# Kernel tuning notes

Hardware: AMD Instinct MI355X
Metric: run time of the kernel (lower is better)

The kernel has to match this reference:

```python
import jax, jax.numpy as jnp
import numpy as np

DIM = 1024
NUM_HEADS = 16


def setup_inputs() -> dict:
    key = jax.random.key(0)
    ks = jax.random.split(key, 8)
    B, N, C = 2, 2048, DIM
    x = jax.random.normal(ks[0], (B, N, C), dtype=jnp.float32)
    attn_mask = jnp.zeros((B, 1, N, N), dtype=jnp.float32)
    # learned parameters
    w_qkv = jax.random.normal(ks[1], (3 * C, C), dtype=jnp.float32) * (C ** -0.5)
    q_bias = jnp.zeros((C,), dtype=jnp.float32)
    k_bias = jnp.zeros((C,), dtype=jnp.float32)
    v_bias = jnp.zeros((C,), dtype=jnp.float32)
    w_proj = jax.random.normal(ks[2], (C, C), dtype=jnp.float32) * (C ** -0.5)
    b_proj = jnp.zeros((C,), dtype=jnp.float32)
    return {
        "x": x, "attn_mask": attn_mask,
        "w_qkv": w_qkv, "q_bias": q_bias, "k_bias": k_bias, "v_bias": v_bias,
        "w_proj": w_proj, "b_proj": b_proj,
        "num_heads": NUM_HEADS,
    }


def reference(x, attn_mask, w_qkv, q_bias, k_bias, v_bias, w_proj, b_proj, num_heads):
    B, N, C = x.shape
    H = num_heads
    hd = C // H
    scale = hd ** -0.5
    alpha = 32.0
    # fused qkv projection with concatenated biases
    qkv_bias = jnp.concatenate([q_bias, k_bias, v_bias])
    qkv = x @ w_qkv.T + qkv_bias                       # [B, N, 3C]
    qkv = qkv.reshape(B, N, 3, H, hd).transpose(2, 0, 3, 1, 4)  # [3, B, H, N, hd]
    q, k, v = qkv[0], qkv[1], qkv[2]
    # stabilization trick: scale q down by alpha, compute scores, re-scale after max-subtraction
    q = q * (scale / alpha)
    attn = jnp.einsum('bhld,bhmd->bhlm', q, k)         # [B, H, N, N]
    attn = (attn - jnp.max(attn, axis=-1, keepdims=True)) * alpha
    attn = attn + attn_mask                            # additive mask, broadcast over heads
    attn = jax.nn.softmax(attn, axis=-1)
    out = jnp.einsum('bhlm,bhmd->blhd', attn, v).reshape(B, N, C)
    out = out @ w_proj.T + b_proj
    return out
```

## Files before the change

kernel.cpp:

```cpp
#include <hip/hip_runtime.h>

typedef unsigned short u16;
typedef __bf16   bf16x8 __attribute__((ext_vector_type(8)));
typedef float    f32x4  __attribute__((ext_vector_type(4)));
typedef unsigned u32x4v __attribute__((ext_vector_type(4)));
typedef u16      u16x8  __attribute__((ext_vector_type(8)));

#define DEV __device__ __forceinline__

DEV u16 f2bf(float f) {
  unsigned u = __float_as_uint(f);
  u += 0x7fffu + ((u >> 16) & 1u);
  return (u16)(u >> 16);
}

DEV f32x4 fzero() { f32x4 z; z[0]=0.f; z[1]=0.f; z[2]=0.f; z[3]=0.f; return z; }

DEV void async_cp16(void* lds, const void* g) {
  __builtin_amdgcn_global_load_lds(
      (const __attribute__((address_space(1))) void*)g,
      (__attribute__((address_space(3))) void*)lds, 16, 0, 0);
}

__global__ void k_cvt_bf16(const float* __restrict__ in, u16* __restrict__ out, int n8) {
  int i = blockIdx.x * blockDim.x + threadIdx.x;
  if (i >= n8) return;
  const float4* in4 = (const float4*)in;
  float4 a = in4[2*i], b = in4[2*i+1];
  u16x8 r;
  r[0]=f2bf(a.x); r[1]=f2bf(a.y); r[2]=f2bf(a.z); r[3]=f2bf(a.w);
  r[4]=f2bf(b.x); r[5]=f2bf(b.y); r[6]=f2bf(b.z); r[7]=f2bf(b.w);
  *(u16x8*)(out + 8*(size_t)i) = r;
}

__global__ void k_zero_flag(unsigned* f) {
  if (threadIdx.x == 0 && blockIdx.x == 0) *f = 0u;
}

__global__ void k_mask_or(const u32x4v* __restrict__ m, int n4, unsigned* __restrict__ f) {
  unsigned o = 0;
  int stride = gridDim.x * blockDim.x;
  for (int i = blockIdx.x * blockDim.x + threadIdx.x; i < n4; i += stride) {
    u32x4v v = m[i];
    o |= v[0] | v[1] | v[2] | v[3];
  }
  if (o & 0x7fffffffu) atomicOr(f, 1u);
}

template<int EPI>
__global__ __launch_bounds__(256)
void k_gemm_nt(const u16* __restrict__ A, const u16* __restrict__ B,
               int N, int K, int nbn,
               const float* __restrict__ bq, const float* __restrict__ bk,
               const float* __restrict__ bv,
               u16* __restrict__ qo, u16* __restrict__ ko, u16* __restrict__ vto,
               float* __restrict__ fo, const float* __restrict__ bp)
{
  __shared__ u16 sA[2][4096];
  __shared__ u16 sB[2][4096];

  const int tid  = threadIdx.x;
  const int lane = tid & 63;
  const int wave = tid >> 6;
  const int lr = lane & 15, lg = lane >> 4;
  const int wr = wave >> 1, wc = wave & 1;

  const int per = gridDim.x >> 3;
  const int bid = blockIdx.x;
  const int swz = (bid & 7) * per + (bid >> 3);
  const int bm0 = (swz / nbn) << 7;
  const int bn0 = (swz - (swz / nbn) * nbn) << 7;

  const size_t Kb = (size_t)K * 2;

  auto stage = [&](int buf, int kt) {
#pragma unroll
    for (int j = 0; j < 2; ++j) {
      int off = (tid + j * 256) << 4;
      int row = off >> 6;
      int ch  = (off & 63) >> 4;
      int gch = ch ^ (row & 3);
      async_cp16((char*)&sA[buf][0] + off,
                 (const char*)A + (size_t)(bm0 + row) * Kb + (size_t)kt * 64 + gch * 16);
      async_cp16((char*)&sB[buf][0] + off,
                 (const char*)B + (size_t)(bn0 + row) * Kb + (size_t)kt * 64 + gch * 16);
    }
  };

  f32x4 acc[4][4];
#pragma unroll
  for (int i = 0; i < 4; ++i)
#pragma unroll
    for (int j = 0; j < 4; ++j) acc[i][j] = fzero();

  const int nk = K >> 5;
  stage(0, 0);
  __syncthreads();

  for (int kt = 0; kt < nk; ++kt) {
    const int cur = kt & 1;
    if (kt + 1 < nk) stage(cur ^ 1, kt + 1);

    bf16x8 af[4], bfr[4];
#pragma unroll
    for (int mi = 0; mi < 4; ++mi) {
      int row = (wr << 6) + (mi << 4) + lr;
      int addr = (row << 6) + ((lg ^ (row & 3)) << 4);
      af[mi] = *(const bf16x8*)((const char*)&sA[cur][0] + addr);
    }
#pragma unroll
    for (int ni = 0; ni < 4; ++ni) {
      int row = (wc << 6) + (ni << 4) + lr;
      int addr = (row << 6) + ((lg ^ (row & 3)) << 4);
      bfr[ni] = *(const bf16x8*)((const char*)&sB[cur][0] + addr);
    }
#pragma unroll
    for (int mi = 0; mi < 4; ++mi)
#pragma unroll
      for (int ni = 0; ni < 4; ++ni)
        acc[mi][ni] = __builtin_amdgcn_mfma_f32_16x16x32_bf16(af[mi], bfr[ni], acc[mi][ni], 0, 0, 0);

    __syncthreads();
  }

#pragma unroll
  for (int mi = 0; mi < 4; ++mi) {
#pragma unroll
    for (int ni = 0; ni < 4; ++ni) {
      int col = bn0 + (wc << 6) + (ni << 4) + lr;
      if (EPI == 0) {
        int s = col >> 10, hd = col & 1023;
        int h = hd >> 6, d = hd & 63;
        float bias = (s == 0 ? bq[hd] : (s == 1 ? bk[hd] : bv[hd]));
#pragma unroll
        for (int r = 0; r < 4; ++r) {
          int m = bm0 + (wr << 6) + (mi << 4) + (lg << 2) + r;
          int b = m >> 11, n = m & 2047;
          u16 val = f2bf(acc[mi][ni][r] + bias);
          size_t bh = (size_t)(b * 16 + h);
          if (s == 0)      qo[(bh * 2048 + n) * 64 + d] = val;
          else if (s == 1) ko[(bh * 2048 + n) * 64 + d] = val;
          else             vto[(bh * 64 + d) * 2048 + n] = val;
        }
      } else {
        float bias = bp[col];
#pragma unroll
        for (int r = 0; r < 4; ++r) {
          int m = bm0 + (wr << 6) + (mi << 4) + (lg << 2) + r;
          fo[(size_t)m * N + col] = acc[mi][ni][r] + bias;
        }
      }
    }
  }
}

__global__ __launch_bounds__(256)
void k_attn(const u16* __restrict__ qb, const u16* __restrict__ kb,
            const u16* __restrict__ vtb, u16* __restrict__ ao,
            const float* __restrict__ mask, const unsigned* __restrict__ flag)
{
  constexpr int N = 2048, D = 64;
  __shared__ u16 sK[2][4096];
  __shared__ u16 sV[2][4096];

  const int tid  = threadIdx.x;
  const int lane = tid & 63;
  const int wave = tid >> 6;
  const int lr = lane & 15, lg = lane >> 4;

  const int bid  = blockIdx.x;
  const int xcd  = bid & 7, slot = bid >> 3;
  const int bh   = xcd + 8 * (slot >> 5);
  const int qt   = slot & 31;
  const int b    = bh >> 4, h = bh & 15;

  const u16* Kbh = kb  + (size_t)bh * N * D;
  const u16* Vbh = vtb + (size_t)bh * D * N;
  const int q_lo = qt * 64 + wave * 16;
  const int qg   = q_lo + lr;

  bf16x8 qf[2];
  {
    const u16* qrow = qb + ((size_t)bh * N + qg) * D;
    qf[0] = *(const bf16x8*)(qrow + lg * 8);
    qf[1] = *(const bf16x8*)(qrow + 32 + lg * 8);
  }

  const unsigned use_mask = *flag;
  const float* maskb = mask + (size_t)b * N * N;

  float m_run = -INFINITY, lsum = 0.f;
  f32x4 o[4];
#pragma unroll
  for (int i = 0; i < 4; ++i) o[i] = fzero();

  auto stage = [&](int buf, int kt) {
#pragma unroll
    for (int j = 0; j < 2; ++j) {
      int off = (tid + j * 256) << 4;
      int row = off >> 7;
      int ch  = (off & 127) >> 4;
      int gch = ch ^ (row & 7);
      async_cp16((char*)&sK[buf][0] + off,
                 (const char*)Kbh + (size_t)(kt * 64 + row) * 128 + gch * 16);
      async_cp16((char*)&sV[buf][0] + off,
                 (const char*)Vbh + (size_t)row * (N * 2) + (size_t)kt * 128 + gch * 16);
    }
  };

  stage(0, 0);
  __syncthreads();

  const float SCALE = 0.125f;
  const float L2E   = 1.44269504088896340736f;

  for (int kt = 0; kt < N / 64; ++kt) {
    const int cur = kt & 1;
    if (kt + 1 < N / 64) stage(cur ^ 1, kt + 1);

    f32x4 sc[4];
#pragma unroll
    for (int mi = 0; mi < 4; ++mi) sc[mi] = fzero();
#pragma unroll
    for (int mi = 0; mi < 4; ++mi)
#pragma unroll
      for (int ks = 0; ks < 2; ++ks) {
        int row = (mi << 4) + lr;
        int addr = (row << 7) + ((((ks << 2) + lg) ^ (row & 7)) << 4);
        bf16x8 kf = *(const bf16x8*)((const char*)&sK[cur][0] + addr);
        sc[mi] = __builtin_amdgcn_mfma_f32_16x16x32_bf16(kf, qf[ks], sc[mi], 0, 0, 0);
      }

    float t[4][4];
#pragma unroll
    for (int mi = 0; mi < 4; ++mi)
#pragma unroll
      for (int r = 0; r < 4; ++r) t[mi][r] = sc[mi][r] * SCALE;

    if (use_mask) {
#pragma unroll
      for (int mi = 0; mi < 4; ++mi)
#pragma unroll
        for (int r = 0; r < 4; ++r) {
          int kg = kt * 64 + (mi << 4) + (lg << 2) + r;
          t[mi][r] += maskb[(size_t)qg * N + kg];
        }
    }

    float pm = t[0][0];
#pragma unroll
    for (int mi = 0; mi < 4; ++mi)
#pragma unroll
      for (int r = 0; r < 4; ++r) pm = fmaxf(pm, t[mi][r]);
    pm = fmaxf(pm, __shfl_xor(pm, 16, 64));
    pm = fmaxf(pm, __shfl_xor(pm, 32, 64));

    const float m_new = fmaxf(m_run, pm);
    const float f = __builtin_amdgcn_exp2f((m_run - m_new) * L2E);
    m_run = m_new;

    float p[4][4];
    float rs = 0.f;
#pragma unroll
    for (int mi = 0; mi < 4; ++mi)
#pragma unroll
      for (int r = 0; r < 4; ++r) {
        p[mi][r] = __builtin_amdgcn_exp2f((t[mi][r] - m_new) * L2E);
        rs += p[mi][r];
      }
    rs += __shfl_xor(rs, 16, 64);
    rs += __shfl_xor(rs, 32, 64);
    lsum = lsum * f + rs;

    {
      float fr[4];
#pragma unroll
      for (int r = 0; r < 4; ++r) fr[r] = __shfl(f, (lg << 2) + r, 64);
#pragma unroll
      for (int ni = 0; ni < 4; ++ni)
#pragma unroll
        for (int r = 0; r < 4; ++r) o[ni][r] *= fr[r];
    }

    unsigned P32[4][2];
#pragma unroll
    for (int mi = 0; mi < 4; ++mi)
#pragma unroll
      for (int rp = 0; rp < 2; ++rp) {
        unsigned lo = f2bf(p[mi][2 * rp]);
        unsigned hi = f2bf(p[mi][2 * rp + 1]);
        P32[mi][rp] = lo | (hi << 16);
      }

    bf16x8 pf[2];
#pragma unroll
    for (int ks = 0; ks < 2; ++ks) {
      u32x4v w;
#pragma unroll
      for (int wd = 0; wd < 4; ++wd) {
        int src = lr + ((((lg << 1) + (wd >> 1)) & 3) << 4);
        unsigned vlo = __shfl(P32[2 * ks + 0][wd & 1], src, 64);
        unsigned vhi = __shfl(P32[2 * ks + 1][wd & 1], src, 64);
        w[wd] = (lg & 2) ? vhi : vlo;
      }
      pf[ks] = __builtin_bit_cast(bf16x8, w);
    }

#pragma unroll
    for (int ni = 0; ni < 4; ++ni)
#pragma unroll
      for (int ks = 0; ks < 2; ++ks) {
        int drow = (ni << 4) + lr;
        int addr = (drow << 7) + ((((ks << 2) + lg) ^ (drow & 7)) << 4);
        bf16x8 vf = *(const bf16x8*)((const char*)&sV[cur][0] + addr);
        o[ni] = __builtin_amdgcn_mfma_f32_16x16x32_bf16(pf[ks], vf, o[ni], 0, 0, 0);
      }

    __syncthreads();
  }

  const float inv = 1.0f / lsum;
  float ivr[4];
#pragma unroll
  for (int r = 0; r < 4; ++r) ivr[r] = __shfl(inv, (lg << 2) + r, 64);

#pragma unroll
  for (int ni = 0; ni < 4; ++ni) {
    int d = (ni << 4) + lr;
#pragma unroll
    for (int r = 0; r < 4; ++r) {
      int qrow = q_lo + (lg << 2) + r;
      ao[((size_t)(b * N + qrow)) * 1024 + h * 64 + d] = f2bf(o[ni][r] * ivr[r]);
    }
  }
}

extern "C" void kernel_launch(void* const* d_in, const int* in_sizes, int n_in,
                              void* d_out, int out_size, void* d_ws, size_t ws_size,
                              hipStream_t stream) {
  const float* x      = (const float*)d_in[0];
  const float* mask   = (const float*)d_in[1];
  const float* w_qkv  = (const float*)d_in[2];
  const float* q_bias = (const float*)d_in[3];
  const float* k_bias = (const float*)d_in[4];
  const float* v_bias = (const float*)d_in[5];
  const float* w_proj = (const float*)d_in[6];
  const float* b_proj = (const float*)d_in[7];
  float* out = (float*)d_out;

  const int B = 2, N = 2048, C = 1024;
  const int M = B * N;

  u16* ws     = (u16*)d_ws;
  u16* xb     = ws;
  u16* wqkvb  = ws + 4194304;
  u16* wprojb = ws + 7340032;
  u16* qbuf   = ws + 8388608;
  u16* kbuf   = ws + 12582912;
  u16* vtbuf  = ws + 16777216;
  unsigned* flag = (unsigned*)(ws + 20971520);
  u16* aob    = xb;

  k_cvt_bf16<<<(M * C / 8 + 255) / 256, 256, 0, stream>>>(x, xb, M * C / 8);
  k_cvt_bf16<<<(3 * C * C / 8 + 255) / 256, 256, 0, stream>>>(w_qkv, wqkvb, 3 * C * C / 8);
  k_cvt_bf16<<<(C * C / 8 + 255) / 256, 256, 0, stream>>>(w_proj, wprojb, C * C / 8);

  k_zero_flag<<<1, 64, 0, stream>>>(flag);
  k_mask_or<<<1024, 256, 0, stream>>>((const u32x4v*)mask, B * N * N / 4, flag);

  k_gemm_nt<0><<<(M / 128) * (3 * C / 128), 256, 0, stream>>>(
      xb, wqkvb, 3 * C, C, 3 * C / 128,
      q_bias, k_bias, v_bias, qbuf, kbuf, vtbuf, nullptr, nullptr);

  k_attn<<<B * 16 * (N / 64), 256, 0, stream>>>(qbuf, kbuf, vtbuf, aob, mask, flag);

  k_gemm_nt<1><<<(M / 128) * (C / 128), 256, 0, stream>>>(
      aob, wprojb, C, C, C / 128,
      nullptr, nullptr, nullptr, nullptr, nullptr, nullptr, out, b_proj);
}
```

Baseline: 174.6 us.

## Fuse preprocessing kernels, fold softmax scale into Q, add lazy rescale and setprio

```diff
diff --git a/kernel.cpp b/kernel.cpp
--- a/kernel.cpp
+++ b/kernel.cpp
@@ -8,10 +8,12 @@
 
 #define DEV __device__ __forceinline__
 
-DEV u16 f2bf(float f) {
-  unsigned u = __float_as_uint(f);
-  u += 0x7fffu + ((u >> 16) & 1u);
-  return (u16)(u >> 16);
+DEV u16 tobf(float f) {
+  return __builtin_bit_cast(unsigned short, (__bf16)f);
+}
+
+DEV unsigned pack2(float a, float b) {
+  return (unsigned)tobf(a) | ((unsigned)tobf(b) << 16);
 }
 
 DEV f32x4 fzero() { f32x4 z; z[0]=0.f; z[1]=0.f; z[2]=0.f; z[3]=0.f; return z; }
@@ -22,14 +24,12 @@
       (__attribute__((address_space(3))) void*)lds, 16, 0, 0);
 }
 
-__global__ void k_cvt_bf16(const float* __restrict__ in, u16* __restrict__ out, int n8) {
-  int i = blockIdx.x * blockDim.x + threadIdx.x;
-  if (i >= n8) return;
+DEV void cvt8(const float* __restrict__ in, u16* __restrict__ out, int i) {
   const float4* in4 = (const float4*)in;
   float4 a = in4[2*i], b = in4[2*i+1];
   u16x8 r;
-  r[0]=f2bf(a.x); r[1]=f2bf(a.y); r[2]=f2bf(a.z); r[3]=f2bf(a.w);
-  r[4]=f2bf(b.x); r[5]=f2bf(b.y); r[6]=f2bf(b.z); r[7]=f2bf(b.w);
+  r[0]=tobf(a.x); r[1]=tobf(a.y); r[2]=tobf(a.z); r[3]=tobf(a.w);
+  r[4]=tobf(b.x); r[5]=tobf(b.y); r[6]=tobf(b.z); r[7]=tobf(b.w);
   *(u16x8*)(out + 8*(size_t)i) = r;
 }
 
@@ -37,14 +37,23 @@
   if (threadIdx.x == 0 && blockIdx.x == 0) *f = 0u;
 }
 
-__global__ void k_mask_or(const u32x4v* __restrict__ m, int n4, unsigned* __restrict__ f) {
+__global__ __launch_bounds__(256)
+void k_pre(const float* __restrict__ x, const float* __restrict__ wqkv,
+           const float* __restrict__ wproj,
+           u16* __restrict__ xb, u16* __restrict__ wqkvb, u16* __restrict__ wprojb,
+           const u32x4v* __restrict__ mask, unsigned* __restrict__ flag)
+{
+  const int tid = blockIdx.x * blockDim.x + threadIdx.x;
+  const int stride = gridDim.x * blockDim.x;
+  for (int i = tid; i < 524288; i += stride) cvt8(x, xb, i);
+  for (int i = tid; i < 393216; i += stride) cvt8(wqkv, wqkvb, i);
+  for (int i = tid; i < 131072; i += stride) cvt8(wproj, wprojb, i);
   unsigned o = 0;
-  int stride = gridDim.x * blockDim.x;
-  for (int i = blockIdx.x * blockDim.x + threadIdx.x; i < n4; i += stride) {
-    u32x4v v = m[i];
+  for (int i = tid; i < 2097152; i += stride) {
+    u32x4v v = mask[i];
     o |= v[0] | v[1] | v[2] | v[3];
   }
-  if (o & 0x7fffffffu) atomicOr(f, 1u);
+  if (o & 0x7fffffffu) atomicOr(flag, 1u);
 }
 
 template<int EPI>
@@ -136,7 +145,9 @@
         for (int r = 0; r < 4; ++r) {
           int m = bm0 + (wr << 6) + (mi << 4) + (lg << 2) + r;
           int b = m >> 11, n = m & 2047;
-          u16 val = f2bf(acc[mi][ni][r] + bias);
+          float v = acc[mi][ni][r] + bias;
+          if (s == 0) v *= 0.125f;
+          u16 val = tobf(v);
           size_t bh = (size_t)(b * 16 + h);
           if (s == 0)      qo[(bh * 2048 + n) * 64 + d] = val;
           else if (s == 1) ko[(bh * 2048 + n) * 64 + d] = val;
@@ -211,8 +222,7 @@
   stage(0, 0);
   __syncthreads();
 
-  const float SCALE = 0.125f;
-  const float L2E   = 1.44269504088896340736f;
+  const float L2E = 1.44269504088896340736f;
 
   for (int kt = 0; kt < N / 64; ++kt) {
     const int cur = kt & 1;
@@ -221,6 +231,7 @@
     f32x4 sc[4];
 #pragma unroll
     for (int mi = 0; mi < 4; ++mi) sc[mi] = fzero();
+    __builtin_amdgcn_s_setprio(1);
 #pragma unroll
     for (int mi = 0; mi < 4; ++mi)
 #pragma unroll
@@ -230,12 +241,7 @@
         bf16x8 kf = *(const bf16x8*)((const char*)&sK[cur][0] + addr);
         sc[mi] = __builtin_amdgcn_mfma_f32_16x16x32_bf16(kf, qf[ks], sc[mi], 0, 0, 0);
       }
-
-    float t[4][4];
-#pragma unroll
-    for (int mi = 0; mi < 4; ++mi)
-#pragma unroll
-      for (int r = 0; r < 4; ++r) t[mi][r] = sc[mi][r] * SCALE;
+    __builtin_amdgcn_s_setprio(0);
 
     if (use_mask) {
 #pragma unroll
@@ -243,54 +249,52 @@
 #pragma unroll
         for (int r = 0; r < 4; ++r) {
           int kg = kt * 64 + (mi << 4) + (lg << 2) + r;
-          t[mi][r] += maskb[(size_t)qg * N + kg];
+          sc[mi][r] += maskb[(size_t)qg * N + kg];
         }
     }
 
-    float pm = t[0][0];
-#pragma unroll
-    for (int mi = 0; mi < 4; ++mi)
-#pragma unroll
-      for (int r = 0; r < 4; ++r) pm = fmaxf(pm, t[mi][r]);
+    float a0 = fmaxf(fmaxf(sc[0][0], sc[0][1]), fmaxf(sc[0][2], sc[0][3]));
+    float a1 = fmaxf(fmaxf(sc[1][0], sc[1][1]), fmaxf(sc[1][2], sc[1][3]));
+    float a2 = fmaxf(fmaxf(sc[2][0], sc[2][1]), fmaxf(sc[2][2], sc[2][3]));
+    float a3 = fmaxf(fmaxf(sc[3][0], sc[3][1]), fmaxf(sc[3][2], sc[3][3]));
+    float pm = fmaxf(fmaxf(a0, a1), fmaxf(a2, a3));
     pm = fmaxf(pm, __shfl_xor(pm, 16, 64));
     pm = fmaxf(pm, __shfl_xor(pm, 32, 64));
 
-    const float m_new = fmaxf(m_run, pm);
-    const float f = __builtin_amdgcn_exp2f((m_run - m_new) * L2E);
-    m_run = m_new;
-
+    if (__any(pm > m_run + 8.f)) {
+      const float m_new = fmaxf(m_run, pm);
+      const float f = __builtin_amdgcn_exp2f((m_run - m_new) * L2E);
+      m_run = m_new;
+      float fr[4];
+#pragma unroll
+      for (int r = 0; r < 4; ++r) fr[r] = __shfl(f, (lg << 2) + r, 64);
+#pragma unroll
+      for (int ni = 0; ni < 4; ++ni)
+#pragma unroll
+        for (int r = 0; r < 4; ++r) o[ni][r] *= fr[r];
+      lsum *= f;
+    }
+
+    const float mL2 = m_run * L2E;
     float p[4][4];
     float rs = 0.f;
 #pragma unroll
     for (int mi = 0; mi < 4; ++mi)
 #pragma unroll
       for (int r = 0; r < 4; ++r) {
-        p[mi][r] = __builtin_amdgcn_exp2f((t[mi][r] - m_new) * L2E);
+        p[mi][r] = __builtin_amdgcn_exp2f(__builtin_fmaf(sc[mi][r], L2E, -mL2));
         rs += p[mi][r];
       }
     rs += __shfl_xor(rs, 16, 64);
     rs += __shfl_xor(rs, 32, 64);
-    lsum = lsum * f + rs;
-
-    {
-      float fr[4];
-#pragma unroll
-      for (int r = 0; r < 4; ++r) fr[r] = __shfl(f, (lg << 2) + r, 64);
-#pragma unroll
-      for (int ni = 0; ni < 4; ++ni)
-#pragma unroll
-        for (int r = 0; r < 4; ++r) o[ni][r] *= fr[r];
-    }
+    lsum += rs;
 
     unsigned P32[4][2];
 #pragma unroll
     for (int mi = 0; mi < 4; ++mi)
 #pragma unroll
-      for (int rp = 0; rp < 2; ++rp) {
-        unsigned lo = f2bf(p[mi][2 * rp]);
-        unsigned hi = f2bf(p[mi][2 * rp + 1]);
-        P32[mi][rp] = lo | (hi << 16);
-      }
+      for (int rp = 0; rp < 2; ++rp)
+        P32[mi][rp] = pack2(p[mi][2 * rp], p[mi][2 * rp + 1]);
 
     bf16x8 pf[2];
 #pragma unroll
@@ -306,6 +310,7 @@
       pf[ks] = __builtin_bit_cast(bf16x8, w);
     }
 
+    __builtin_amdgcn_s_setprio(1);
 #pragma unroll
     for (int ni = 0; ni < 4; ++ni)
 #pragma unroll
@@ -315,6 +320,7 @@
         bf16x8 vf = *(const bf16x8*)((const char*)&sV[cur][0] + addr);
         o[ni] = __builtin_amdgcn_mfma_f32_16x16x32_bf16(pf[ks], vf, o[ni], 0, 0, 0);
       }
+    __builtin_amdgcn_s_setprio(0);
 
     __syncthreads();
   }
@@ -330,7 +336,7 @@
 #pragma unroll
     for (int r = 0; r < 4; ++r) {
       int qrow = q_lo + (lg << 2) + r;
-      ao[((size_t)(b * N + qrow)) * 1024 + h * 64 + d] = f2bf(o[ni][r] * ivr[r]);
+      ao[((size_t)(b * N + qrow)) * 1024 + h * 64 + d] = tobf(o[ni][r] * ivr[r]);
     }
   }
 }
@@ -361,12 +367,9 @@
   unsigned* flag = (unsigned*)(ws + 20971520);
   u16* aob    = xb;
 
-  k_cvt_bf16<<<(M * C / 8 + 255) / 256, 256, 0, stream>>>(x, xb, M * C / 8);
-  k_cvt_bf16<<<(3 * C * C / 8 + 255) / 256, 256, 0, stream>>>(w_qkv, wqkvb, 3 * C * C / 8);
-  k_cvt_bf16<<<(C * C / 8 + 255) / 256, 256, 0, stream>>>(w_proj, wprojb, C * C / 8);
-
   k_zero_flag<<<1, 64, 0, stream>>>(flag);
-  k_mask_or<<<1024, 256, 0, stream>>>((const u32x4v*)mask, B * N * N / 4, flag);
+  k_pre<<<2048, 256, 0, stream>>>(x, w_qkv, w_proj, xb, wqkvb, wprojb,
+                                  (const u32x4v*)mask, flag);
 
   k_gemm_nt<0><<<(M / 128) * (3 * C / 128), 256, 0, stream>>>(
       xb, wqkvb, 3 * C, C, 3 * C / 128,
```

After: 159.5 us. -8.7%, faster.
